# Kernel optimization log

Measured on AMD Instinct MI355X. Metric: run time of the kernel, lower is better.

The kernel has to match this reference:

```python
import jax, jax.numpy as jnp
import numpy as np

B, H, N, D = 2, 16, 2048, 128

def setup_inputs() -> dict:
    key = jax.random.key(0)
    kq, kk, kv = jax.random.split(key, 3)
    q = jax.random.normal(kq, (B, H, N, D), dtype=jnp.float32)
    k = jax.random.normal(kk, (B, H, N, D), dtype=jnp.float32)
    v = jax.random.normal(kv, (B, H, N, D), dtype=jnp.float32)
    return {"q": q, "k": k, "v": v}

def reference(q, k, v):
    # scale = 1/sqrt(d) computed at forward time (scale=None in __init__)
    d = q.shape[-1]
    scale = 1.0 / jnp.sqrt(jnp.asarray(d, dtype=q.dtype))
    # scores: (B, H, N, N)
    scores = jnp.einsum('bhnd,bhmd->bhnm', q, k) * scale
    probs = jax.nn.softmax(scores, axis=-1)
    return jnp.einsum('bhnm,bhmd->bhnd', probs, v)
```

## Files before the change

### kernel.cpp

```cpp
#include <hip/hip_runtime.h>
#include <hip/hip_fp16.h>

#define BH   32
#define SEQ  2048
#define DIM  128
#define CK   32
#define NCH  (SEQ / CK)

typedef _Float16 half8   __attribute__((ext_vector_type(8)));
typedef __fp16   fp16x2  __attribute__((ext_vector_type(2)));
typedef _Float16 half2v  __attribute__((ext_vector_type(2)));
typedef float    floatx4 __attribute__((ext_vector_type(4)));

__device__ inline half2v pk2(float a, float b) {
    fp16x2 t = __builtin_amdgcn_cvt_pkrtz(a, b);
    return *(half2v*)&t;
}
__device__ inline half8 pk8(float4 a, float4 b) {
    half2v l0 = pk2(a.x, a.y), l1 = pk2(a.z, a.w);
    half2v l2 = pk2(b.x, b.y), l3 = pk2(b.z, b.w);
    half8 h;
    h[0] = l0[0]; h[1] = l0[1]; h[2] = l1[0]; h[3] = l1[1];
    h[4] = l2[0]; h[5] = l2[1]; h[6] = l3[0]; h[7] = l3[1];
    return h;
}

__device__ inline void ld16(const void* g, void* l) {
    __builtin_amdgcn_global_load_lds(
        (__attribute__((address_space(1))) void*)(uintptr_t)g,
        (__attribute__((address_space(3))) void*)(uintptr_t)l, 16, 0, 0);
}

#define SYNC_VM(N) do {                                        \
    asm volatile("s_waitcnt vmcnt(" #N ")" ::: "memory");      \
    __builtin_amdgcn_s_barrier();                              \
    asm volatile("" ::: "memory");                             \
} while (0)

__global__ void prep_kernel(const float* __restrict__ k, const float* __restrict__ v,
                            _Float16* __restrict__ kh, _Float16* __restrict__ vt) {
    const float SC = 0.08838834764831845f * 1.4426950408889634f;
    __shared__ __align__(16) _Float16 t[32][136];
    const int bh = blockIdx.x >> 6;
    const int kc = blockIdx.x & 63;
    const int tid = threadIdx.x;
    const size_t base = ((size_t)bh * SEQ + kc * CK) * DIM;

    const float4* kf4 = (const float4*)(k + base);
    const float4* vf4 = (const float4*)(v + base);
    half8* kh8 = (half8*)(kh + base);

    #pragma unroll
    for (int i = 0; i < 2; i++) {
        int f8 = i * 256 + tid;
        float4 a = kf4[2 * f8], b = kf4[2 * f8 + 1];
        a.x *= SC; a.y *= SC; a.z *= SC; a.w *= SC;
        b.x *= SC; b.y *= SC; b.z *= SC; b.w *= SC;
        kh8[f8] = pk8(a, b);
        int row = f8 >> 4, c8 = f8 & 15;
        *((half8*)&t[row][c8 * 8]) = pk8(vf4[2 * f8], vf4[2 * f8 + 1]);
    }
    __syncthreads();
    _Float16* vout = vt + ((size_t)bh * NCH + kc) * (DIM * CK);
    #pragma unroll
    for (int i = 0; i < 2; i++) {
        int g = i * 256 + tid;
        int d = g >> 2, kg = g & 3;
        half8 h;
        #pragma unroll
        for (int j = 0; j < 8; j++) h[j] = t[kg * 8 + j][d];
        *((half8*)(vout + d * CK + kg * 8)) = h;
    }
}

__global__ __launch_bounds__(256, 2) void attn_kernel(
        const float* __restrict__ q, const _Float16* __restrict__ kh,
        const _Float16* __restrict__ vt, float* __restrict__ out) {
    __shared__ __align__(16) _Float16 Kbuf[3][CK * DIM];
    __shared__ __align__(16) _Float16 Vbuf[3][DIM * CK];
    __shared__ __align__(16) _Float16 Pld[4][2][16][40];

    const int lid = blockIdx.x + (blockIdx.y << 4);
    const int xcd = lid & 7;
    const int idx = lid >> 3;
    const int bh  = (xcd << 2) + (idx >> 4);
    const int qt  = idx & 15;

    const int tid  = threadIdx.x;
    const int w    = tid >> 6;
    const int lane = tid & 63;
    const int l15  = lane & 15;
    const int quad = lane >> 4;

    half8 qf[2][4];
    #pragma unroll
    for (int s = 0; s < 2; s++) {
        const float* qb = q + ((size_t)bh * SEQ + qt * 128 + w * 32 + s * 16 + l15) * DIM;
        #pragma unroll
        for (int c = 0; c < 4; c++) {
            float4 a = *((const float4*)(qb + c * 32 + quad * 8));
            float4 b = *((const float4*)(qb + c * 32 + quad * 8 + 4));
            qf[s][c] = pk8(a, b);
        }
    }

    half8 ones;
    #pragma unroll
    for (int j = 0; j < 8; j++) ones[j] = (_Float16)1.0f;

    floatx4 zf = {0.f, 0.f, 0.f, 0.f};
    floatx4 O[2][8];
    #pragma unroll
    for (int s = 0; s < 2; s++)
        #pragma unroll
        for (int i = 0; i < 8; i++) O[s][i] = zf;
    floatx4 Osum[2] = {zf, zf};

    const _Float16* kb = kh + (size_t)bh * SEQ * DIM;
    const _Float16* vb = vt + (size_t)bh * SEQ * DIM;

    const int s0 = w * 128 + lane;
    const int s1 = s0 + 64;
    const int kr0 = s0 >> 4, kg0 = ((s0 & 15) - kr0) & 15;
    const int kr1 = s1 >> 4, kg1 = ((s1 & 15) - kr1) & 15;
    const _Float16* kgp0 = kb + kr0 * DIM + kg0 * 8;
    const _Float16* kgp1 = kb + kr1 * DIM + kg1 * 8;
    const _Float16* vgp0 = vb + s0 * 8;
    const _Float16* vgp1 = vb + s1 * 8;

    auto dma = [&](int kc, int b) {
        size_t off = (size_t)kc * (CK * DIM);
        ld16(kgp0 + off, &Kbuf[b][(w * 2 + 0) * 512]);
        ld16(kgp1 + off, &Kbuf[b][(w * 2 + 1) * 512]);
        ld16(vgp0 + off, &Vbuf[b][(w * 2 + 0) * 512]);
        ld16(vgp1 + off, &Vbuf[b][(w * 2 + 1) * 512]);
    };

    const int row0 = 2 * l15, row1 = 2 * l15 + 1;

    auto chunk = [&](int cb) {
        const _Float16* Kc = Kbuf[cb];
        const _Float16* Vc = Vbuf[cb];

        floatx4 S[2][2];
        #pragma unroll
        for (int s = 0; s < 2; s++) { S[s][0] = zf; S[s][1] = zf; }
        __builtin_amdgcn_s_setprio(1);
        #pragma unroll
        for (int c = 0; c < 4; c++) {
            int g = c * 4 + quad;
            half8 b0 = *((const half8*)&Kc[row0 * DIM + (((g + row0) & 15) * 8)]);
            half8 b1 = *((const half8*)&Kc[row1 * DIM + (((g + row1) & 15) * 8)]);
            #pragma unroll
            for (int s = 0; s < 2; s++) {
                S[s][0] = __builtin_amdgcn_mfma_f32_16x16x32_f16(qf[s][c], b0, S[s][0], 0, 0, 0);
                S[s][1] = __builtin_amdgcn_mfma_f32_16x16x32_f16(qf[s][c], b1, S[s][1], 0, 0, 0);
            }
        }
        __builtin_amdgcn_s_setprio(0);

        half8 vfr[8];
        #pragma unroll
        for (int dt = 0; dt < 8; dt++)
            vfr[dt] = *((const half8*)&Vc[(dt * 16 + l15) * CK + quad * 8]);

        #pragma unroll
        for (int s = 0; s < 2; s++)
            #pragma unroll
            for (int r = 0; r < 4; r++) {
                float p0 = exp2f(S[s][0][r]);
                float p1 = exp2f(S[s][1][r]);
                *((half2v*)&Pld[w][s][quad * 4 + r][2 * l15]) = pk2(p0, p1);
            }

        half8 pf0 = *((const half8*)&Pld[w][0][l15][quad * 8]);
        half8 pf1 = *((const half8*)&Pld[w][1][l15][quad * 8]);

        __builtin_amdgcn_s_setprio(1);
        Osum[0] = __builtin_amdgcn_mfma_f32_16x16x32_f16(pf0, ones, Osum[0], 0, 0, 0);
        Osum[1] = __builtin_amdgcn_mfma_f32_16x16x32_f16(pf1, ones, Osum[1], 0, 0, 0);
        #pragma unroll
        for (int dt = 0; dt < 8; dt++) {
            O[0][dt] = __builtin_amdgcn_mfma_f32_16x16x32_f16(pf0, vfr[dt], O[0][dt], 0, 0, 0);
            O[1][dt] = __builtin_amdgcn_mfma_f32_16x16x32_f16(pf1, vfr[dt], O[1][dt], 0, 0, 0);
        }
        __builtin_amdgcn_s_setprio(0);
    };

    dma(0, 0);
    dma(1, 1);

    int c0 = 0;
    #pragma unroll 3
    for (int kc = 0; kc < NCH - 1; kc++) {
        SYNC_VM(4);
        if (kc + 2 < NCH) {
            int c2 = c0 + 2; if (c2 >= 3) c2 -= 3;
            dma(kc + 2, c2);
        }
        chunk(c0);
        c0 = (c0 == 2) ? 0 : c0 + 1;
    }
    SYNC_VM(0);
    chunk(c0);

    #pragma unroll
    for (int s = 0; s < 2; s++) {
        float* ob = out + ((size_t)bh * SEQ + qt * 128 + w * 32 + s * 16) * DIM;
        #pragma unroll
        for (int r = 0; r < 4; r++) {
            float rinv = 1.0f / Osum[s][r];
            #pragma unroll
            for (int dt = 0; dt < 8; dt++) {
                ob[(size_t)(quad * 4 + r) * DIM + dt * 16 + l15] = O[s][dt][r] * rinv;
            }
        }
    }
}

extern "C" void kernel_launch(void* const* d_in, const int* in_sizes, int n_in,
                              void* d_out, int out_size, void* d_ws, size_t ws_size,
                              hipStream_t stream) {
    const float* q = (const float*)d_in[0];
    const float* k = (const float*)d_in[1];
    const float* v = (const float*)d_in[2];
    float* out = (float*)d_out;

    const size_t elems = (size_t)BH * SEQ * DIM;
    _Float16* kh = (_Float16*)d_ws;
    _Float16* vtp = kh + elems;

    prep_kernel<<<BH * NCH, 256, 0, stream>>>(k, v, kh, vtp);
    attn_kernel<<<dim3(SEQ / 128, BH), 256, 0, stream>>>(q, kh, vtp, out);
}
```

Measured before the change: 214.0 us.

## Software-pipeline PV MFMAs one chunk behind QK and re-swizzle LDS layouts

The attention loop is restructured so each iteration runs the QK^T MFMAs for chunk kc while the PV MFMAs use the probabilities from chunk kc-1. The P fragment is read back from LDS at the end of the iteration, so the LDS round-trip latency overlaps other work. V gets a fourth ring buffer (the spare one zeroed so the first iteration's dummy PV adds nothing), plus a new LDS layout for V and a new K swizzle (stride 3 per row pair) aimed at fewer bank conflicts. It also switches to the raw exp2 intrinsic, at the cost of more LDS, longer register live ranges and a hand-written epilogue.

```diff
diff --git a/kernel.cpp b/kernel.cpp
--- a/kernel.cpp
+++ b/kernel.cpp
@@ -77,7 +77,7 @@
         const float* __restrict__ q, const _Float16* __restrict__ kh,
         const _Float16* __restrict__ vt, float* __restrict__ out) {
     __shared__ __align__(16) _Float16 Kbuf[3][CK * DIM];
-    __shared__ __align__(16) _Float16 Vbuf[3][DIM * CK];
+    __shared__ __align__(16) _Float16 Vbuf[4][DIM * CK];
     __shared__ __align__(16) _Float16 Pld[4][2][16][40];
 
     const int lid = blockIdx.x + (blockIdx.y << 4);
@@ -92,6 +92,13 @@
     const int l15  = lane & 15;
     const int quad = lane >> 4;
 
+    {
+        float4 z4 = {0.f, 0.f, 0.f, 0.f};
+        ((float4*)&Vbuf[3][0])[tid] = z4;
+        ((float4*)&Vbuf[3][0])[tid + 256] = z4;
+        asm volatile("s_waitcnt lgkmcnt(0)" ::: "memory");
+    }
+
     half8 qf[2][4];
     #pragma unroll
     for (int s = 0; s < 2; s++) {
@@ -121,88 +128,154 @@
 
     const int s0 = w * 128 + lane;
     const int s1 = s0 + 64;
-    const int kr0 = s0 >> 4, kg0 = ((s0 & 15) - kr0) & 15;
-    const int kr1 = s1 >> 4, kg1 = ((s1 & 15) - kr1) & 15;
+    const int kr0 = s0 >> 4, kg0 = ((s0 & 15) - 3 * (kr0 >> 1)) & 15;
+    const int kr1 = s1 >> 4, kg1 = ((s1 & 15) - 3 * (kr1 >> 1)) & 15;
     const _Float16* kgp0 = kb + kr0 * DIM + kg0 * 8;
     const _Float16* kgp1 = kb + kr1 * DIM + kg1 * 8;
-    const _Float16* vgp0 = vb + s0 * 8;
-    const _Float16* vgp1 = vb + s1 * 8;
-
-    auto dma = [&](int kc, int b) {
+    const int vo0 = ((s0 >> 6) * 16 + (s0 & 15)) * CK + ((s0 >> 4) & 3) * 8;
+    const int vo1 = ((s1 >> 6) * 16 + (s1 & 15)) * CK + ((s1 >> 4) & 3) * 8;
+    const _Float16* vgp0 = vb + vo0;
+    const _Float16* vgp1 = vb + vo1;
+
+    auto dma = [&](int kc, int bk, int bv) {
         size_t off = (size_t)kc * (CK * DIM);
-        ld16(kgp0 + off, &Kbuf[b][(w * 2 + 0) * 512]);
-        ld16(kgp1 + off, &Kbuf[b][(w * 2 + 1) * 512]);
-        ld16(vgp0 + off, &Vbuf[b][(w * 2 + 0) * 512]);
-        ld16(vgp1 + off, &Vbuf[b][(w * 2 + 1) * 512]);
+        ld16(kgp0 + off, &Kbuf[bk][(w * 2 + 0) * 512]);
+        ld16(kgp1 + off, &Kbuf[bk][(w * 2 + 1) * 512]);
+        ld16(vgp0 + off, &Vbuf[bv][(w * 2 + 0) * 512]);
+        ld16(vgp1 + off, &Vbuf[bv][(w * 2 + 1) * 512]);
     };
 
     const int row0 = 2 * l15, row1 = 2 * l15 + 1;
 
-    auto chunk = [&](int cb) {
-        const _Float16* Kc = Kbuf[cb];
-        const _Float16* Vc = Vbuf[cb];
-
-        floatx4 S[2][2];
-        #pragma unroll
-        for (int s = 0; s < 2; s++) { S[s][0] = zf; S[s][1] = zf; }
-        __builtin_amdgcn_s_setprio(1);
-        #pragma unroll
-        for (int c = 0; c < 4; c++) {
-            int g = c * 4 + quad;
-            half8 b0 = *((const half8*)&Kc[row0 * DIM + (((g + row0) & 15) * 8)]);
-            half8 b1 = *((const half8*)&Kc[row1 * DIM + (((g + row1) & 15) * 8)]);
-            #pragma unroll
-            for (int s = 0; s < 2; s++) {
-                S[s][0] = __builtin_amdgcn_mfma_f32_16x16x32_f16(qf[s][c], b0, S[s][0], 0, 0, 0);
-                S[s][1] = __builtin_amdgcn_mfma_f32_16x16x32_f16(qf[s][c], b1, S[s][1], 0, 0, 0);
-            }
-        }
-        __builtin_amdgcn_s_setprio(0);
-
-        half8 vfr[8];
-        #pragma unroll
-        for (int dt = 0; dt < 8; dt++)
-            vfr[dt] = *((const half8*)&Vc[(dt * 16 + l15) * CK + quad * 8]);
-
-        #pragma unroll
-        for (int s = 0; s < 2; s++)
-            #pragma unroll
-            for (int r = 0; r < 4; r++) {
-                float p0 = exp2f(S[s][0][r]);
-                float p1 = exp2f(S[s][1][r]);
-                *((half2v*)&Pld[w][s][quad * 4 + r][2 * l15]) = pk2(p0, p1);
-            }
-
-        half8 pf0 = *((const half8*)&Pld[w][0][l15][quad * 8]);
-        half8 pf1 = *((const half8*)&Pld[w][1][l15][quad * 8]);
-
-        __builtin_amdgcn_s_setprio(1);
-        Osum[0] = __builtin_amdgcn_mfma_f32_16x16x32_f16(pf0, ones, Osum[0], 0, 0, 0);
-        Osum[1] = __builtin_amdgcn_mfma_f32_16x16x32_f16(pf1, ones, Osum[1], 0, 0, 0);
-        #pragma unroll
-        for (int dt = 0; dt < 8; dt++) {
-            O[0][dt] = __builtin_amdgcn_mfma_f32_16x16x32_f16(pf0, vfr[dt], O[0][dt], 0, 0, 0);
-            O[1][dt] = __builtin_amdgcn_mfma_f32_16x16x32_f16(pf1, vfr[dt], O[1][dt], 0, 0, 0);
-        }
-        __builtin_amdgcn_s_setprio(0);
-    };
-
-    dma(0, 0);
-    dma(1, 1);
-
-    int c0 = 0;
+    half8 pf0, pf1;
+    #pragma unroll
+    for (int j = 0; j < 8; j++) { pf0[j] = (_Float16)0.0f; pf1[j] = (_Float16)0.0f; }
+
+    dma(0, 0, 0);
+    dma(1, 1, 1);
+
+    int bk = 0;
     #pragma unroll 3
     for (int kc = 0; kc < NCH - 1; kc++) {
         SYNC_VM(4);
         if (kc + 2 < NCH) {
-            int c2 = c0 + 2; if (c2 >= 3) c2 -= 3;
-            dma(kc + 2, c2);
-        }
-        chunk(c0);
-        c0 = (c0 == 2) ? 0 : c0 + 1;
-    }
+            int bk2 = bk + 2; if (bk2 >= 3) bk2 -= 3;
+            dma(kc + 2, bk2, (kc + 2) & 3);
+        }
+
+        const _Float16* Kc = Kbuf[bk];
+
+        floatx4 S[2][2];
+        #pragma unroll
+        for (int s = 0; s < 2; s++) { S[s][0] = zf; S[s][1] = zf; }
+        __builtin_amdgcn_s_setprio(1);
+        #pragma unroll
+        for (int c = 0; c < 4; c++) {
+            int P = ((c * 4 + quad) + 3 * l15) & 15;
+            half8 b0 = *((const half8*)&Kc[row0 * DIM + P * 8]);
+            half8 b1 = *((const half8*)&Kc[row1 * DIM + P * 8]);
+            #pragma unroll
+            for (int s = 0; s < 2; s++) {
+                S[s][0] = __builtin_amdgcn_mfma_f32_16x16x32_f16(qf[s][c], b0, S[s][0], 0, 0, 0);
+                S[s][1] = __builtin_amdgcn_mfma_f32_16x16x32_f16(qf[s][c], b1, S[s][1], 0, 0, 0);
+            }
+        }
+        __builtin_amdgcn_s_setprio(0);
+
+        const _Float16* Vp = Vbuf[(kc + 3) & 3];
+        half8 vfr[8];
+        #pragma unroll
+        for (int dt = 0; dt < 8; dt++)
+            vfr[dt] = *((const half8*)&Vp[dt * 512 + (quad * 16 + l15) * 8]);
+
+        #pragma unroll
+        for (int s = 0; s < 2; s++)
+            #pragma unroll
+            for (int r = 0; r < 4; r++) {
+                float p0 = __builtin_amdgcn_exp2f(S[s][0][r]);
+                float p1 = __builtin_amdgcn_exp2f(S[s][1][r]);
+                *((half2v*)&Pld[w][s][quad * 4 + r][2 * l15]) = pk2(p0, p1);
+            }
+
+        __builtin_amdgcn_s_setprio(1);
+        Osum[0] = __builtin_amdgcn_mfma_f32_16x16x32_f16(pf0, ones, Osum[0], 0, 0, 0);
+        Osum[1] = __builtin_amdgcn_mfma_f32_16x16x32_f16(pf1, ones, Osum[1], 0, 0, 0);
+        #pragma unroll
+        for (int dt = 0; dt < 8; dt++) {
+            O[0][dt] = __builtin_amdgcn_mfma_f32_16x16x32_f16(pf0, vfr[dt], O[0][dt], 0, 0, 0);
+            O[1][dt] = __builtin_amdgcn_mfma_f32_16x16x32_f16(pf1, vfr[dt], O[1][dt], 0, 0, 0);
+        }
+        __builtin_amdgcn_s_setprio(0);
+
+        pf0 = *((const half8*)&Pld[w][0][l15][quad * 8]);
+        pf1 = *((const half8*)&Pld[w][1][l15][quad * 8]);
+
+        bk++; if (bk == 3) bk = 0;
+    }
+
     SYNC_VM(0);
-    chunk(c0);
+    {
+        const _Float16* Kc = Kbuf[bk];
+        floatx4 S[2][2];
+        #pragma unroll
+        for (int s = 0; s < 2; s++) { S[s][0] = zf; S[s][1] = zf; }
+        __builtin_amdgcn_s_setprio(1);
+        #pragma unroll
+        for (int c = 0; c < 4; c++) {
+            int P = ((c * 4 + quad) + 3 * l15) & 15;
+            half8 b0 = *((const half8*)&Kc[row0 * DIM + P * 8]);
+            half8 b1 = *((const half8*)&Kc[row1 * DIM + P * 8]);
+            #pragma unroll
+            for (int s = 0; s < 2; s++) {
+                S[s][0] = __builtin_amdgcn_mfma_f32_16x16x32_f16(qf[s][c], b0, S[s][0], 0, 0, 0);
+                S[s][1] = __builtin_amdgcn_mfma_f32_16x16x32_f16(qf[s][c], b1, S[s][1], 0, 0, 0);
+            }
+        }
+        __builtin_amdgcn_s_setprio(0);
+
+        const _Float16* Vp = Vbuf[(NCH + 2) & 3];
+        half8 vfr[8];
+        #pragma unroll
+        for (int dt = 0; dt < 8; dt++)
+            vfr[dt] = *((const half8*)&Vp[dt * 512 + (quad * 16 + l15) * 8]);
+
+        #pragma unroll
+        for (int s = 0; s < 2; s++)
+            #pragma unroll
+            for (int r = 0; r < 4; r++) {
+                float p0 = __builtin_amdgcn_exp2f(S[s][0][r]);
+                float p1 = __builtin_amdgcn_exp2f(S[s][1][r]);
+                *((half2v*)&Pld[w][s][quad * 4 + r][2 * l15]) = pk2(p0, p1);
+            }
+
+        __builtin_amdgcn_s_setprio(1);
+        Osum[0] = __builtin_amdgcn_mfma_f32_16x16x32_f16(pf0, ones, Osum[0], 0, 0, 0);
+        Osum[1] = __builtin_amdgcn_mfma_f32_16x16x32_f16(pf1, ones, Osum[1], 0, 0, 0);
+        #pragma unroll
+        for (int dt = 0; dt < 8; dt++) {
+            O[0][dt] = __builtin_amdgcn_mfma_f32_16x16x32_f16(pf0, vfr[dt], O[0][dt], 0, 0, 0);
+            O[1][dt] = __builtin_amdgcn_mfma_f32_16x16x32_f16(pf1, vfr[dt], O[1][dt], 0, 0, 0);
+        }
+        __builtin_amdgcn_s_setprio(0);
+
+        pf0 = *((const half8*)&Pld[w][0][l15][quad * 8]);
+        pf1 = *((const half8*)&Pld[w][1][l15][quad * 8]);
+
+        const _Float16* Vl = Vbuf[(NCH - 1) & 3];
+        half8 vfl[8];
+        #pragma unroll
+        for (int dt = 0; dt < 8; dt++)
+            vfl[dt] = *((const half8*)&Vl[dt * 512 + (quad * 16 + l15) * 8]);
+        __builtin_amdgcn_s_setprio(1);
+        Osum[0] = __builtin_amdgcn_mfma_f32_16x16x32_f16(pf0, ones, Osum[0], 0, 0, 0);
+        Osum[1] = __builtin_amdgcn_mfma_f32_16x16x32_f16(pf1, ones, Osum[1], 0, 0, 0);
+        #pragma unroll
+        for (int dt = 0; dt < 8; dt++) {
+            O[0][dt] = __builtin_amdgcn_mfma_f32_16x16x32_f16(pf0, vfl[dt], O[0][dt], 0, 0, 0);
+            O[1][dt] = __builtin_amdgcn_mfma_f32_16x16x32_f16(pf1, vfl[dt], O[1][dt], 0, 0, 0);
+        }
+        __builtin_amdgcn_s_setprio(0);
+    }
 
     #pragma unroll
     for (int s = 0; s < 2; s++) {
```

New measurement: 203.0 us. 5.1% less time.
